# Kernel optimization log

Measured on AMD Instinct MI355X. Metric: run time of the kernel, lower is better.

## Reference

```python
import jax, jax.numpy as jnp
import numpy as np

N = 50000          # nodes
E = 800000         # edges (avg degree 16)
D = 128            # feature dim
MSG_EPS = 1e-7     # GENConv eps added to relu(msg)
SM_EPS = 1e-16     # pyg softmax denominator eps
BN_EPS = 1e-5
LN_EPS = 1e-5


def setup_inputs() -> dict:
    key = jax.random.key(0)
    ks = jax.random.split(key, 6)
    x = jax.random.normal(ks[0], (N, D), dtype=jnp.float32)
    edge_index = jax.random.randint(ks[1], (2, E), 0, N, dtype=jnp.int32)
    t = jnp.array(1.0, dtype=jnp.float32)
    W1 = jax.random.normal(ks[2], (D, 2 * D), dtype=jnp.float32) / np.sqrt(D).astype(np.float32)
    b1 = jnp.zeros((2 * D,), jnp.float32)
    bn_gamma = jnp.ones((2 * D,), jnp.float32)
    bn_beta = jnp.zeros((2 * D,), jnp.float32)
    W2 = jax.random.normal(ks[3], (2 * D, D), dtype=jnp.float32) / np.sqrt(2 * D).astype(np.float32)
    b2 = jnp.zeros((D,), jnp.float32)
    ln_gamma = jnp.ones((D,), jnp.float32)
    ln_beta = jnp.zeros((D,), jnp.float32)
    return {"x": x, "edge_index": edge_index, "t": t, "W1": W1, "b1": b1,
            "bn_gamma": bn_gamma, "bn_beta": bn_beta, "W2": W2, "b2": b2,
            "ln_gamma": ln_gamma, "ln_beta": ln_beta}


def reference(x, edge_index, t, W1, b1, bn_gamma, bn_beta, W2, b2, ln_gamma, ln_beta):
    src, dst = edge_index[0], edge_index[1]
    # --- GENConv message: relu(x_j) + eps  -> [E, D]
    msg = jax.nn.relu(x[src]) + MSG_EPS
    # --- softmax aggregation over incoming edges per dst node, per feature
    logits = t * msg                                            # [E, D]
    seg_max = jax.ops.segment_max(logits, dst, num_segments=N)  # [N, D]
    seg_max = jnp.where(jnp.isfinite(seg_max), seg_max, 0.0)    # empty segments -> 0
    ex = jnp.exp(logits - seg_max[dst])                         # [E, D]
    denom = jax.ops.segment_sum(ex, dst, num_segments=N)        # [N, D]
    alpha = ex / (denom[dst] + SM_EPS)                          # [E, D]
    agg = jax.ops.segment_sum(alpha * msg, dst, num_segments=N) # [N, D]
    # --- GENConv update: MLP(agg + x), MLP = Lin(D,2D)->BN->ReLU->Lin(2D,D)
    h = agg + x
    h = h @ W1 + b1                                             # [N, 2D]
    mu = jnp.mean(h, axis=0)
    var = jnp.var(h, axis=0)
    h = (h - mu) * jax.lax.rsqrt(var + BN_EPS) * bn_gamma + bn_beta
    h = jax.nn.relu(h)
    h = h @ W2 + b2                                             # [N, D]
    # --- LayerNorm -> ReLU -> (dropout p=0 noop) -> residual
    mu2 = jnp.mean(h, axis=-1, keepdims=True)
    var2 = jnp.mean(jnp.square(h - mu2), axis=-1, keepdims=True)
    h = (h - mu2) * jax.lax.rsqrt(var2 + LN_EPS) * ln_gamma + ln_beta
    h = jax.nn.relu(h)
    return x + h
```

## Files before the change

### kernel.cpp

```cpp
#include <hip/hip_runtime.h>

#define D 128
#define D2 256
#define BSH 5
#define BNODES 32
#define NBMAX 2048
#define CAP 640
#define PCHUNK 8192
#define REP 32
#define CSTRIDE 16
#define ZWORDS (2 * REP * 256 + NBMAX * CSTRIDE)

typedef __attribute__((ext_vector_type(8))) short short8;
typedef __attribute__((ext_vector_type(4))) float f32x4;

__device__ inline unsigned short f2b(float f) {
  unsigned u = __float_as_uint(f);
  unsigned r = (u + 0x7FFFu + ((u >> 16) & 1u)) >> 16;
  return (unsigned short)r;
}
__device__ inline float lo2f(unsigned u) { return __uint_as_float(u << 16); }
__device__ inline float hi2f(unsigned u) { return __uint_as_float(u & 0xffff0000u); }

__global__ __launch_bounds__(256) void prep_kernel(
    const float* __restrict__ x, const float* __restrict__ W1,
    const float* __restrict__ W2, const float* __restrict__ tptr,
    unsigned short* __restrict__ mb,
    unsigned short* __restrict__ W1f, unsigned short* __restrict__ W2f,
    float* __restrict__ zbase, int total4) {
  int idx = blockIdx.x * 256 + threadIdx.x;
  if (idx < 32768) {
    int k = idx >> 8, n = idx & 255;
    int t = n >> 4, m16 = n & 15;
    int kk = k >> 5, quad = (k >> 3) & 3, j = k & 7;
    W1f[(((t * 4 + kk) * 64 + quad * 16 + m16) << 3) + j] = f2b(W1[idx]);
  } else if (idx < 65536) {
    int i = idx - 32768;
    int k = i >> 7, n = i & 127;
    int t = n >> 4, m16 = n & 15;
    int kk = k >> 5, quad = (k >> 3) & 3, j = k & 7;
    W2f[(((t * 8 + kk) * 64 + quad * 16 + m16) << 3) + j] = f2b(W2[i]);
  } else if (idx < 65536 + total4) {
    int i = idx - 65536;
    float scl = tptr[0] * 1.4426950408889634f;
    float4 v = reinterpret_cast<const float4*>(x)[i];
    unsigned lo = (unsigned)f2b(scl * (fmaxf(v.x, 0.f) + 1e-7f)) |
                  ((unsigned)f2b(scl * (fmaxf(v.y, 0.f) + 1e-7f)) << 16);
    unsigned hi = (unsigned)f2b(scl * (fmaxf(v.z, 0.f) + 1e-7f)) |
                  ((unsigned)f2b(scl * (fmaxf(v.w, 0.f) + 1e-7f)) << 16);
    reinterpret_cast<uint2*>(mb)[i] = make_uint2(lo, hi);
  } else if (idx < 65536 + total4 + 32) {
    reinterpret_cast<uint2*>(mb)[idx - 65536] = make_uint2(0u, 0u);
  } else if (idx < 65536 + total4 + 32 + ZWORDS) {
    zbase[idx - (65536 + total4 + 32)] = 0.f;
  }
}

__global__ __launch_bounds__(256) void part_kernel(const int* __restrict__ ei,
                                                   int* __restrict__ cursor,
                                                   unsigned* __restrict__ pairbuf,
                                                   int E, int nb) {
  __shared__ int cnt[NBMAX];
  __shared__ int base[NBMAX];
  int tid = threadIdx.x;
  int c0 = blockIdx.x * PCHUNK;
  int nE = min(PCHUNK, E - c0);
  for (int i = tid; i < nb; i += 256) cnt[i] = 0;
  __syncthreads();
  for (int j = tid; j < nE; j += 256) {
    int dst = ei[E + c0 + j];
    atomicAdd(&cnt[dst >> BSH], 1);
  }
  __syncthreads();
  for (int i = tid; i < nb; i += 256) {
    int c = cnt[i];
    base[i] = (c > 0) ? atomicAdd(&cursor[i * CSTRIDE], c) : 0;
    cnt[i] = 0;
  }
  __syncthreads();
  for (int j = tid; j < nE; j += 256) {
    int e = c0 + j;
    int dst = ei[E + e];
    int src = ei[e];
    int b = dst >> BSH;
    int r = base[b] + atomicAdd(&cnt[b], 1);
    if (r < CAP)
      pairbuf[(size_t)b * CAP + r] =
          (unsigned)src | ((unsigned)(dst & (BNODES - 1)) << 16);
  }
}

__global__ __launch_bounds__(512) void agg2_kernel(const float* __restrict__ x,
                                                   const unsigned short* __restrict__ mb,
                                                   const unsigned* __restrict__ pairbuf,
                                                   const int* __restrict__ cursor,
                                                   const float* __restrict__ tptr,
                                                   unsigned short* __restrict__ h0b, int N) {
  __shared__ int soff[CAP + 4 * BNODES];
  __shared__ int cnt[BNODES], off[BNODES], run[BNODES], pcnt[BNODES];
  int b = blockIdx.x;
  int tid = threadIdx.x;
  int Eb = min(cursor[b * CSTRIDE], CAP);
  if (tid < BNODES) { cnt[tid] = 0; run[tid] = 0; }
  __syncthreads();
  for (int j = tid; j < Eb; j += 512)
    atomicAdd(&cnt[pairbuf[(size_t)b * CAP + j] >> 16], 1);
  __syncthreads();
  if (tid < BNODES) {
    int c = cnt[tid];
    int pc = (c + 3) & ~3;
    pcnt[tid] = pc;
    int s = pc;
#pragma unroll
    for (int st = 1; st < 32; st <<= 1) {
      int u = __shfl_up(s, st, 32);
      if ((tid & 31) >= st) s += u;
    }
    off[tid] = s - pc;
  }
  __syncthreads();
  for (int j = tid; j < Eb; j += 512) {
    unsigned p = pairbuf[(size_t)b * CAP + j];
    int dl = p >> 16;
    int r = atomicAdd(&run[dl], 1);
    soff[off[dl] + r] = (int)(p & 0xffffu) << 8;
  }
  if (tid < BNODES) {
    int o = off[tid];
    for (int r = cnt[tid]; r < pcnt[tid]; ++r) soff[o + r] = N << 8;
  }
  __syncthreads();

  int w = tid >> 6;
  int l = tid & 63;
  int half = l >> 5;
  int l32 = l & 31;
  float numscale = 0.69314718055994531f / tptr[0];
  int laneoff = l32 << 3;
  const char* mbase = (const char*)mb;

#define PROC(W)                                        \
  do {                                                 \
    float u0 = lo2f((W).x), u1 = hi2f((W).x);          \
    float u2 = lo2f((W).y), u3 = hi2f((W).y);          \
    float e0, e1, e2, e3;                              \
    asm("v_exp_f32 %0, %1" : "=v"(e0) : "v"(u0));      \
    asm("v_exp_f32 %0, %1" : "=v"(e1) : "v"(u1));      \
    asm("v_exp_f32 %0, %1" : "=v"(e2) : "v"(u2));      \
    asm("v_exp_f32 %0, %1" : "=v"(e3) : "v"(u3));      \
    den0 += e0; num0 = fmaf(e0, u0, num0);             \
    den1 += e1; num1 = fmaf(e1, u1, num1);             \
    den2 += e2; num2 = fmaf(e2, u2, num2);             \
    den3 += e3; num3 = fmaf(e3, u3, num3);             \
  } while (0)

#pragma unroll
  for (int p = 0; p < 2; ++p) {
    int ln = (p << 4) | (w << 1) | half;
    int n = (b << BSH) + ln;
    if (n >= N) continue;
    int s0 = off[ln];
    int dn = pcnt[ln];
    size_t idx = ((size_t)n << 7) + (l32 << 2);
    float4 xv = *reinterpret_cast<const float4*>(x + idx);
    float den0 = 0.f, num0 = 0.f, den1 = 0.f, num1 = 0.f;
    float den2 = 0.f, num2 = 0.f, den3 = 0.f, num3 = 0.f;
    if (dn > 0) {
      uint2 uu[4];
#pragma unroll
      for (int q = 0; q < 4; ++q)
        uu[q] = *(const uint2*)(mbase + (soff[s0 + q] | laneoff));
      for (int j = 4; j < dn; j += 4) {
        uint2 vv[4];
#pragma unroll
        for (int q = 0; q < 4; ++q)
          vv[q] = *(const uint2*)(mbase + (soff[s0 + j + q] | laneoff));
#pragma unroll
        for (int q = 0; q < 4; ++q) PROC(uu[q]);
#pragma unroll
        for (int q = 0; q < 4; ++q) uu[q] = vv[q];
      }
#pragma unroll
      for (int q = 0; q < 4; ++q) PROC(uu[q]);
      float fnpad = (float)(dn - cnt[ln]);
      den0 -= fnpad; den1 -= fnpad; den2 -= fnpad; den3 -= fnpad;
    }
    float v0 = num0 * numscale / (den0 + 1e-16f) + xv.x;
    float v1 = num1 * numscale / (den1 + 1e-16f) + xv.y;
    float v2 = num2 * numscale / (den2 + 1e-16f) + xv.z;
    float v3 = num3 * numscale / (den3 + 1e-16f) + xv.w;
    uint2 o;
    o.x = (unsigned)f2b(v0) | ((unsigned)f2b(v1) << 16);
    o.y = (unsigned)f2b(v2) | ((unsigned)f2b(v3) << 16);
    *reinterpret_cast<uint2*>(h0b + idx) = o;
  }
#undef PROC
}

__global__ __launch_bounds__(256) void gemm1_stats(
    const unsigned short* __restrict__ h0b, const unsigned short* __restrict__ W1f,
    float* __restrict__ bnsum, float* __restrict__ bnsumsq, int M) {
  int tid = threadIdx.x;
  int w = tid >> 6;
  int l = tid & 63;
  int m16 = l & 15;
  int quad = l >> 4;
  int r0 = blockIdx.x * 64;

  f32x4 acc[4][4];
#pragma unroll
  for (int rt = 0; rt < 4; ++rt)
#pragma unroll
    for (int ct = 0; ct < 4; ++ct) acc[rt][ct] = (f32x4){0.f, 0.f, 0.f, 0.f};

#pragma unroll
  for (int kk = 0; kk < 4; ++kk) {
    short8 bfr[4];
#pragma unroll
    for (int ct = 0; ct < 4; ++ct)
      bfr[ct] = *reinterpret_cast<const short8*>(
          W1f + ((((w * 4 + ct) * 4 + kk) * 64 + l) << 3));
    short8 a[4];
#pragma unroll
    for (int rt = 0; rt < 4; ++rt) {
      int row = min(r0 + rt * 16 + m16, M - 1);
      a[rt] = *reinterpret_cast<const short8*>(h0b + (size_t)row * D + kk * 32 + quad * 8);
    }
#pragma unroll
    for (int rt = 0; rt < 4; ++rt)
#pragma unroll
      for (int ct = 0; ct < 4; ++ct)
        acc[rt][ct] = __builtin_amdgcn_mfma_f32_16x16x32_bf16(a[rt], bfr[ct], acc[rt][ct], 0, 0, 0);
  }

  int rep = (blockIdx.x & (REP - 1)) << 8;
#pragma unroll
  for (int ct = 0; ct < 4; ++ct) {
    int col = w * 64 + ct * 16 + m16;
    float cs = 0.f, cq = 0.f;
#pragma unroll
    for (int rt = 0; rt < 4; ++rt) {
      int rloc = rt * 16 + quad * 4;
#pragma unroll
      for (int reg = 0; reg < 4; ++reg) {
        float val = acc[rt][ct][reg];
        if (r0 + rloc + reg < M) {
          cs += val;
          cq += val * val;
        }
      }
    }
    cs += __shfl_xor(cs, 16, 64);
    cs += __shfl_xor(cs, 32, 64);
    cq += __shfl_xor(cq, 16, 64);
    cq += __shfl_xor(cq, 32, 64);
    if (quad == 0) {
      atomicAdd(&bnsum[rep + col], cs);
      atomicAdd(&bnsumsq[rep + col], cq);
    }
  }
}

__global__ __launch_bounds__(256) void gemm2_mfma(
    const unsigned short* __restrict__ h0b, const unsigned short* __restrict__ W1f,
    const unsigned short* __restrict__ W2f, const float* __restrict__ b2,
    const float* __restrict__ bnsum, const float* __restrict__ bnsumsq,
    const float* __restrict__ bng, const float* __restrict__ bnb,
    const float* __restrict__ lng, const float* __restrict__ lnb,
    const float* __restrict__ x, float* __restrict__ out, int M) {
  __shared__ unsigned short lt[4][64][72];
  __shared__ float lnp[64][2], lnp2[64][2];
  __shared__ float sS[D2], sH[D2];
  int tid = threadIdx.x;
  {
    float s = 0.f, q = 0.f;
#pragma unroll
    for (int r = 0; r < REP; ++r) {
      s += bnsum[(r << 8) + tid];
      q += bnsumsq[(r << 8) + tid];
    }
    float invM = 1.f / (float)M;
    float mu = s * invM;
    float var = q * invM - mu * mu;
    float sc = bng[tid] * rsqrtf(var + 1e-5f);
    sS[tid] = sc;
    sH[tid] = bnb[tid] - mu * sc;
  }
  __syncthreads();

  int w = tid >> 6;
  int l = tid & 63;
  int m16 = l & 15;
  int quad = l >> 4;
  int r0 = blockIdx.x * 64;

  {
    f32x4 acc[4][4];
#pragma unroll
    for (int rt = 0; rt < 4; ++rt)
#pragma unroll
      for (int ct = 0; ct < 4; ++ct) acc[rt][ct] = (f32x4){0.f, 0.f, 0.f, 0.f};

#pragma unroll
    for (int kk = 0; kk < 4; ++kk) {
      short8 bfr[4];
#pragma unroll
      for (int ct = 0; ct < 4; ++ct)
        bfr[ct] = *reinterpret_cast<const short8*>(
            W1f + ((((w * 4 + ct) * 4 + kk) * 64 + l) << 3));
      short8 a[4];
#pragma unroll
      for (int rt = 0; rt < 4; ++rt) {
        int row = min(r0 + rt * 16 + m16, M - 1);
        a[rt] = *reinterpret_cast<const short8*>(h0b + (size_t)row * D + kk * 32 + quad * 8);
      }
#pragma unroll
      for (int rt = 0; rt < 4; ++rt)
#pragma unroll
        for (int ct = 0; ct < 4; ++ct)
          acc[rt][ct] = __builtin_amdgcn_mfma_f32_16x16x32_bf16(a[rt], bfr[ct], acc[rt][ct], 0, 0, 0);
    }

#pragma unroll
    for (int ct = 0; ct < 4; ++ct) {
      int col = w * 64 + ct * 16 + m16;
      float sc = sS[col];
      float sh = sH[col];
#pragma unroll
      for (int rt = 0; rt < 4; ++rt) {
        int rloc = rt * 16 + quad * 4;
#pragma unroll
        for (int reg = 0; reg < 4; ++reg) {
          float h = fmaxf(acc[rt][ct][reg] * sc + sh, 0.f);
          lt[w][rloc + reg][ct * 16 + m16] = f2b(h);
        }
      }
    }
  }
  __syncthreads();

  int rb = w >> 1, cb = w & 1;
  f32x4 acc[2][4];
#pragma unroll
  for (int rt = 0; rt < 2; ++rt)
#pragma unroll
    for (int ct = 0; ct < 4; ++ct) acc[rt][ct] = (f32x4){0.f, 0.f, 0.f, 0.f};

#pragma unroll
  for (int kk = 0; kk < 8; ++kk) {
    int base = kk * 32 + quad * 8;
    short8 a[2];
#pragma unroll
    for (int rt = 0; rt < 2; ++rt) {
      int rl = rb * 32 + rt * 16 + m16;
      a[rt] = *reinterpret_cast<const short8*>(&lt[base >> 6][rl][base & 63]);
    }
    short8 bfr[4];
#pragma unroll
    for (int ct = 0; ct < 4; ++ct)
      bfr[ct] = *reinterpret_cast<const short8*>(
          W2f + ((((cb * 4 + ct) * 8 + kk) * 64 + l) << 3));
#pragma unroll
    for (int rt = 0; rt < 2; ++rt)
#pragma unroll
      for (int ct = 0; ct < 4; ++ct)
        acc[rt][ct] = __builtin_amdgcn_mfma_f32_16x16x32_bf16(a[rt], bfr[ct], acc[rt][ct], 0, 0, 0);
  }

  float b2v[4], lgv[4], lbv[4];
#pragma unroll
  for (int ct = 0; ct < 4; ++ct) {
    int col = cb * 64 + ct * 16 + m16;
    b2v[ct] = b2[col];
    lgv[ct] = lng[col];
    lbv[ct] = lnb[col];
  }

#pragma unroll
  for (int rt = 0; rt < 2; ++rt) {
#pragma unroll
    for (int reg = 0; reg < 4; ++reg) {
      float s = 0.f, s2 = 0.f;
#pragma unroll
      for (int ct = 0; ct < 4; ++ct) {
        float v = acc[rt][ct][reg] + b2v[ct];
        s += v;
        s2 += v * v;
      }
#pragma unroll
      for (int msk = 1; msk < 16; msk <<= 1) {
        s += __shfl_xor(s, msk, 64);
        s2 += __shfl_xor(s2, msk, 64);
      }
      if (m16 == 0) {
        int rl = rb * 32 + rt * 16 + quad * 4 + reg;
        lnp[rl][cb] = s;
        lnp2[rl][cb] = s2;
      }
    }
  }
  __syncthreads();

#pragma unroll
  for (int rt = 0; rt < 2; ++rt) {
#pragma unroll
    for (int reg = 0; reg < 4; ++reg) {
      int rl = rb * 32 + rt * 16 + quad * 4 + reg;
      int row = r0 + rl;
      float s = lnp[rl][0] + lnp[rl][1];
      float s2 = lnp2[rl][0] + lnp2[rl][1];
      float mu = s * (1.f / 128.f);
      float var = s2 * (1.f / 128.f) - mu * mu;
      float inv = rsqrtf(var + 1e-5f);
      if (row < M) {
#pragma unroll
        for (int ct = 0; ct < 4; ++ct) {
          int col = cb * 64 + ct * 16 + m16;
          float v = acc[rt][ct][reg] + b2v[ct];
          float h = fmaxf((v - mu) * inv * lgv[ct] + lbv[ct], 0.f);
          out[(size_t)row * D + col] = x[(size_t)row * D + col] + h;
        }
      }
    }
  }
}

extern "C" void kernel_launch(void* const* d_in, const int* in_sizes, int n_in,
                              void* d_out, int out_size, void* d_ws, size_t ws_size,
                              hipStream_t stream) {
  const float* x   = (const float*)d_in[0];
  const int*   ei  = (const int*)d_in[1];
  const float* t   = (const float*)d_in[2];
  const float* W1  = (const float*)d_in[3];
  const float* bng = (const float*)d_in[5];
  const float* bnb = (const float*)d_in[6];
  const float* W2  = (const float*)d_in[7];
  const float* b2  = (const float*)d_in[8];
  const float* lng = (const float*)d_in[9];
  const float* lnb = (const float*)d_in[10];
  float* out = (float*)d_out;

  int N = in_sizes[0] / D;
  int E = in_sizes[1] / 2;
  size_t nd = (size_t)N * D;
  int nb = (N + BNODES - 1) >> BSH;

  unsigned short* mb  = (unsigned short*)d_ws;
  unsigned short* h0b = mb + nd + 128;
  unsigned short* W1f = h0b + nd;
  unsigned short* W2f = W1f + 32768;
  float* bnsum   = (float*)(W2f + 32768);
  float* bnsumsq = bnsum + REP * 256;
  int* cursor    = (int*)(bnsumsq + REP * 256);
  unsigned* pairbuf = (unsigned*)(cursor + NBMAX * CSTRIDE);

  int total4 = (int)(nd / 4);
  int ptotal = 65536 + total4 + 32 + ZWORDS;
  prep_kernel<<<(ptotal + 255) / 256, 256, 0, stream>>>(x, W1, W2, t, mb, W1f, W2f,
                                                        bnsum, total4);

  part_kernel<<<(E + PCHUNK - 1) / PCHUNK, 256, 0, stream>>>(ei, cursor, pairbuf, E, nb);
  agg2_kernel<<<nb, 512, 0, stream>>>(x, mb, pairbuf, cursor, t, h0b, N);

  gemm1_stats<<<(N + 63) / 64, 256, 0, stream>>>(h0b, W1f, bnsum, bnsumsq, N);
  gemm2_mfma<<<(N + 63) / 64, 256, 0, stream>>>(h0b, W1f, W2f, b2, bnsum, bnsumsq,
                                                bng, bnb, lng, lnb, x, out, N);
}
```

Measured before the change: 209.1 us.

## Replace atomic-cursor edge partition with histogram, scan, and deterministic scatter

The single partition kernel reserved per-bucket slots with global atomics on a padded cursor array. It is replaced by three kernels: a per-block bucket histogram, a column-wise exclusive scan across 256 edge blocks that gives each block fixed start offsets and per-bucket totals, and a scatter that writes pairs at those offsets. This removes global atomic contention and makes slot placement deterministic, and drops the cursor zeroing in the prep kernel. The cost is two extra launches, reading the edge array twice, and 256x2048 histogram and start tables in the workspace.

```diff
diff --git a/kernel.cpp b/kernel.cpp
--- a/kernel.cpp
+++ b/kernel.cpp
@@ -6,10 +6,9 @@
 #define BNODES 32
 #define NBMAX 2048
 #define CAP 640
-#define PCHUNK 8192
+#define EBLK 256
 #define REP 32
-#define CSTRIDE 16
-#define ZWORDS (2 * REP * 256 + NBMAX * CSTRIDE)
+#define ZWORDS (2 * REP * 256)
 
 typedef __attribute__((ext_vector_type(8))) short short8;
 typedef __attribute__((ext_vector_type(4))) float f32x4;
@@ -56,34 +55,64 @@
   }
 }
 
-__global__ __launch_bounds__(256) void part_kernel(const int* __restrict__ ei,
-                                                   int* __restrict__ cursor,
-                                                   unsigned* __restrict__ pairbuf,
+__global__ __launch_bounds__(256) void hist_kernel(const int* __restrict__ ei,
+                                                   int* __restrict__ hist,
                                                    int E, int nb) {
   __shared__ int cnt[NBMAX];
-  __shared__ int base[NBMAX];
-  int tid = threadIdx.x;
-  int c0 = blockIdx.x * PCHUNK;
-  int nE = min(PCHUNK, E - c0);
+  int tid = threadIdx.x, blk = blockIdx.x;
+  int per = (E + EBLK - 1) / EBLK;
+  int c0 = blk * per;
+  int nE = min(per, E - c0);
   for (int i = tid; i < nb; i += 256) cnt[i] = 0;
   __syncthreads();
-  for (int j = tid; j < nE; j += 256) {
-    int dst = ei[E + c0 + j];
-    atomicAdd(&cnt[dst >> BSH], 1);
-  }
-  __syncthreads();
-  for (int i = tid; i < nb; i += 256) {
-    int c = cnt[i];
-    base[i] = (c > 0) ? atomicAdd(&cursor[i * CSTRIDE], c) : 0;
-    cnt[i] = 0;
-  }
-  __syncthreads();
+  for (int j = tid; j < nE; j += 256)
+    atomicAdd(&cnt[ei[E + c0 + j] >> BSH], 1);
+  __syncthreads();
+  for (int i = tid; i < nb; i += 256) hist[blk * nb + i] = cnt[i];
+}
+
+__global__ __launch_bounds__(256) void scan_kernel(const int* __restrict__ hist,
+                                                   int* __restrict__ start,
+                                                   int* __restrict__ total, int nb) {
+  __shared__ int wsum[4];
+  int b = blockIdx.x;
+  int t = threadIdx.x;
+  int l = t & 63, w = t >> 6;
+  int v = hist[t * nb + b];
+  int s = v;
+#pragma unroll
+  for (int st = 1; st < 64; st <<= 1) {
+    int u = __shfl_up(s, st, 64);
+    if (l >= st) s += u;
+  }
+  if (l == 63) wsum[w] = s;
+  __syncthreads();
+  int base = 0;
+#pragma unroll
+  for (int i = 0; i < 4; ++i)
+    if (i < w) base += wsum[i];
+  start[t * nb + b] = base + s - v;
+  if (t == 255) total[b] = base + s;
+}
+
+__global__ __launch_bounds__(256) void scatc_kernel(const int* __restrict__ ei,
+                                                    const int* __restrict__ start,
+                                                    unsigned* __restrict__ pairbuf,
+                                                    int E, int nb) {
+  __shared__ int run[NBMAX];
+  int tid = threadIdx.x, blk = blockIdx.x;
+  int per = (E + EBLK - 1) / EBLK;
+  int c0 = blk * per;
+  int nE = min(per, E - c0);
+  for (int i = tid; i < nb; i += 256) run[i] = 0;
+  __syncthreads();
+  const int* srow = start + blk * nb;
   for (int j = tid; j < nE; j += 256) {
     int e = c0 + j;
     int dst = ei[E + e];
     int src = ei[e];
     int b = dst >> BSH;
-    int r = base[b] + atomicAdd(&cnt[b], 1);
+    int r = srow[b] + atomicAdd(&run[b], 1);
     if (r < CAP)
       pairbuf[(size_t)b * CAP + r] =
           (unsigned)src | ((unsigned)(dst & (BNODES - 1)) << 16);
@@ -93,14 +122,14 @@
 __global__ __launch_bounds__(512) void agg2_kernel(const float* __restrict__ x,
                                                    const unsigned short* __restrict__ mb,
                                                    const unsigned* __restrict__ pairbuf,
-                                                   const int* __restrict__ cursor,
+                                                   const int* __restrict__ total,
                                                    const float* __restrict__ tptr,
                                                    unsigned short* __restrict__ h0b, int N) {
   __shared__ int soff[CAP + 4 * BNODES];
   __shared__ int cnt[BNODES], off[BNODES], run[BNODES], pcnt[BNODES];
   int b = blockIdx.x;
   int tid = threadIdx.x;
-  int Eb = min(cursor[b * CSTRIDE], CAP);
+  int Eb = min(total[b], CAP);
   if (tid < BNODES) { cnt[tid] = 0; run[tid] = 0; }
   __syncthreads();
   for (int j = tid; j < Eb; j += 512)
@@ -451,16 +480,20 @@
   unsigned short* W2f = W1f + 32768;
   float* bnsum   = (float*)(W2f + 32768);
   float* bnsumsq = bnsum + REP * 256;
-  int* cursor    = (int*)(bnsumsq + REP * 256);
-  unsigned* pairbuf = (unsigned*)(cursor + NBMAX * CSTRIDE);
+  int* total     = (int*)(bnsumsq + REP * 256);
+  int* hist      = total + NBMAX;
+  int* startb    = hist + EBLK * NBMAX;
+  unsigned* pairbuf = (unsigned*)(startb + EBLK * NBMAX);
 
   int total4 = (int)(nd / 4);
   int ptotal = 65536 + total4 + 32 + ZWORDS;
   prep_kernel<<<(ptotal + 255) / 256, 256, 0, stream>>>(x, W1, W2, t, mb, W1f, W2f,
                                                         bnsum, total4);
 
-  part_kernel<<<(E + PCHUNK - 1) / PCHUNK, 256, 0, stream>>>(ei, cursor, pairbuf, E, nb);
-  agg2_kernel<<<nb, 512, 0, stream>>>(x, mb, pairbuf, cursor, t, h0b, N);
+  hist_kernel<<<EBLK, 256, 0, stream>>>(ei, hist, E, nb);
+  scan_kernel<<<nb, 256, 0, stream>>>(hist, startb, total, nb);
+  scatc_kernel<<<EBLK, 256, 0, stream>>>(ei, startb, pairbuf, E, nb);
+  agg2_kernel<<<nb, 512, 0, stream>>>(x, mb, pairbuf, total, t, h0b, N);
 
   gemm1_stats<<<(N + 63) / 64, 256, 0, stream>>>(h0b, W1f, bnsum, bnsumsq, N);
   gemm2_mfma<<<(N + 63) / 64, 256, 0, stream>>>(h0b, W1f, W2f, b2, bnsum, bnsumsq,
```

Result: faster. 204.3 us (-2.3%).
